# Performance work log

Hardware: AMD Instinct MI355X
Metric: run time of the kernel (lower is better)

Reference implementation:

```python
import jax, jax.numpy as jnp
import numpy as np

B, NUM_CLASSES, H, W, CF = 2, 19, 64, 64, 256
TOPK_IDX = 20  # hard-coded in the torch source: sorted descending value at index 20


def _cosine(x):
    # x: [B, N, D] -> clamped cosine affinity [B, N, N]
    xn = x / (jnp.linalg.norm(x, axis=2, keepdims=True) + 1e-9)
    return jnp.maximum(jnp.einsum('bnd,bmd->bnm', xn, xn), 0.0)


def _conv1x1(x, w, b):
    # x: [B, C, H, W], w: [O, C], b: [O]
    return jnp.einsum('bchw,oc->bohw', x, w) + b[None, :, None, None]


def setup_inputs() -> dict:
    key = jax.random.key(0)
    ks = jax.random.split(key, 12)
    s_c = (2.0 / NUM_CLASSES) ** 0.5  # kaiming fan_in scale for 1x1 conv
    s_f = (2.0 / CF) ** 0.5
    return {
        'pred': jax.random.normal(ks[0], (B, NUM_CLASSES, H, W), jnp.float32),
        'feat': jax.random.normal(ks[1], (B, CF, H, W), jnp.float32),
        'w_cls1': jax.random.normal(ks[2], (NUM_CLASSES, NUM_CLASSES), jnp.float32) * s_c,
        'b_cls1': jnp.zeros((NUM_CLASSES,), jnp.float32),
        'w_cls2': jax.random.normal(ks[3], (NUM_CLASSES, NUM_CLASSES), jnp.float32) * s_c,
        'b_cls2': jnp.zeros((NUM_CLASSES,), jnp.float32),
        'w_pro1': jax.random.normal(ks[4], (CF, CF), jnp.float32) * s_f,
        'b_pro1': jnp.zeros((CF,), jnp.float32),
        'w_pro2': jax.random.normal(ks[5], (CF, CF), jnp.float32) * s_f,
        'b_pro2': jnp.zeros((CF,), jnp.float32),
        'class_weight': jnp.ones((NUM_CLASSES,), jnp.float32),
    }


def reference(pred, feat, w_cls1, b_cls1, w_cls2, b_cls2,
              w_pro1, b_pro1, w_pro2, b_pro2, class_weight):
    bsz, c, h, w = feat.shape
    C = pred.shape[1]
    N = h * w
    feat_flat = feat.reshape(bsz, c, N).transpose(0, 2, 1)  # [B, N, 256]

    # --- no_grad block 1: confidence mask + top-k sparsified cosine affinity ---
    prob = jax.nn.softmax(pred, axis=1)
    p_prob = prob.max(axis=1)      # [B, H, W]
    p_max = prob.argmax(axis=1)    # [B, H, W]
    cwm = class_weight / (class_weight.max() + 1e-10) * 0.95
    mask = ((p_prob >= 0.95) | (p_prob >= cwm[p_max])).astype(jnp.float32)
    mask = jax.lax.stop_gradient(mask.reshape(bsz, N, 1))  # broadcast over classes

    aff1 = _cosine(feat_flat)                                # [B, N, N]
    thr = -jnp.sort(-aff1, axis=-1)[:, :, TOPK_IDX:TOPK_IDX + 1]  # per-row 21st largest
    aff1 = jnp.where(aff1 < thr, 0.0, aff1)
    aff1 = jax.lax.stop_gradient(aff1 + aff1.transpose(0, 2, 1))

    # --- degree-normalized propagation of predictions ---
    pred_flat = pred.reshape(bsz, C, N).transpose(0, 2, 1)   # [B, N, C]
    d1 = (aff1.sum(-1) + 1e-10) ** -0.5                      # D^{-1/2}
    aff1n = d1[:, :, None] * aff1 * d1[:, None, :]           # D^{-1/2} A D^{-1/2}
    p2 = jnp.einsum('bnm,bmc->bnc', aff1n, pred_flat)
    p3 = (0.8 * p2 + 0.2 * pred_flat) * (1.0 - mask) + (0.2 * p2 + 0.8 * pred_flat) * mask
    pred2 = p3.transpose(0, 2, 1).reshape(bsz, C, h, w)
    pred_out = _conv1x1(_conv1x1(pred2, w_cls1, b_cls1), w_cls2, b_cls2)

    # --- no_grad block 2: class-consistency-masked affinity over refined softmax ---
    oh = jax.nn.one_hot(p_max, C, dtype=jnp.float32)         # [B, H, W, C]
    # faithful to torch: permute(0,2,3,1) on the already-[B,H,W,C] one-hot, then flat view
    oh = jnp.transpose(oh, (0, 2, 3, 1)).reshape(bsz, -1, C)
    sp = jax.nn.softmax(pred_out, axis=1).reshape(bsz, C, N).transpose(0, 2, 1)
    aff_f = _cosine(sp)
    aff_f = jnp.where(_cosine(oh) == 0.0, 0.0, aff_f)
    d2 = (aff_f.sum(-1) + 1e-10) ** -0.5
    aff_fn = jax.lax.stop_gradient(d2[:, :, None] * aff_f * d2[:, None, :])

    # --- propagate features and project ---
    new_feat = jnp.einsum('bnm,bmc->bnc', aff_fn, feat_flat)
    new_feat = new_feat.transpose(0, 2, 1).reshape(bsz, c, h, w)
    feat_out = _conv1x1(jax.nn.relu(_conv1x1(new_feat, w_pro1, b_pro1)), w_pro2, b_pro2)
    return pred_out, feat_out
```

## Files before the change

### kernel.cpp

```cpp
#include <hip/hip_runtime.h>

#define NN 4096
#define DD 256
#define CC 19
#define BB 2
#define KSPLIT 4

typedef __attribute__((ext_vector_type(8))) short bf16x8;
typedef _Float16 f16x8 __attribute__((ext_vector_type(8)));
typedef __attribute__((ext_vector_type(4))) float f32x4;

__device__ inline unsigned short f2b(float f) {
  unsigned int u = __float_as_uint(f);
  return (unsigned short)((u + 0x7FFFu + ((u >> 16) & 1u)) >> 16);
}
__device__ inline float b2f(unsigned short h) {
  return __uint_as_float(((unsigned int)h) << 16);
}
__device__ inline unsigned int pack2(float a, float b) {
  return (unsigned int)f2b(a) | ((unsigned int)f2b(b) << 16);
}
__device__ inline void split16(float x, unsigned short& h, unsigned short& l) {
  _Float16 hh = (_Float16)x;
  float hf = (float)hh;
  _Float16 ll = (_Float16)((x - hf) * 2048.0f);
  h = *reinterpret_cast<unsigned short*>(&hh);
  l = *reinterpret_cast<unsigned short*>(&ll);
}

__global__ void k_mask_bits(const float* __restrict__ pred, const float* __restrict__ cw,
                            float* __restrict__ maskb, unsigned int* __restrict__ ohbits) {
  int g = blockIdx.x * 256 + threadIdx.x;
  if (g >= BB * NN) return;
  int b = g >> 12, n = g & (NN - 1);
  const float* p = pred + (size_t)b * CC * NN + n;
  float v[CC];
  float mx = -1e30f; int am = 0;
#pragma unroll
  for (int c = 0; c < CC; ++c) {
    float t = p[(size_t)c * NN];
    v[c] = t;
    if (t > mx) { mx = t; am = c; }
  }
  float s = 0.f;
#pragma unroll
  for (int c = 0; c < CC; ++c) s += expf(v[c] - mx);
  float pprob = 1.f / s;
  float cmax = 0.f;
#pragma unroll
  for (int c = 0; c < CC; ++c) cmax = fmaxf(cmax, cw[c]);
  float cwm = cw[am] / (cmax + 1e-10f) * 0.95f;
  maskb[g] = (pprob >= 0.95f || pprob >= cwm) ? 1.f : 0.f;
  int h = n >> 6, w = n & 63;
  int L = w * (CC * 64) + am * 64 + h;
  atomicOr(&ohbits[b * NN + L / CC], 1u << (L % CC));
}

__global__ void k_norm_feat(const float* __restrict__ feat,
                            unsigned short* __restrict__ xh, unsigned short* __restrict__ xl) {
  int g = blockIdx.x * 64 + threadIdx.x;
  int b = g >> 12, n = g & (NN - 1);
  const float* f = feat + (size_t)b * DD * NN + n;
  float s = 0.f;
  for (int d = 0; d < DD; ++d) { float t = f[(size_t)d * NN]; s += t * t; }
  float r = 1.f / (sqrtf(s) + 1e-9f);
  size_t ob = ((size_t)b * NN + n) * DD;
  for (int d = 0; d < DD; d += 4) {
    ushort4 oh, ol;
    split16(f[(size_t)d * NN] * r, oh.x, ol.x);
    split16(f[(size_t)(d + 1) * NN] * r, oh.y, ol.y);
    split16(f[(size_t)(d + 2) * NN] * r, oh.z, ol.z);
    split16(f[(size_t)(d + 3) * NN] * r, oh.w, ol.w);
    *reinterpret_cast<ushort4*>(&xh[ob + d]) = oh;
    *reinterpret_cast<ushort4*>(&xl[ob + d]) = ol;
  }
}

__global__ __launch_bounds__(256, 2) void k_gram1(const unsigned short* __restrict__ xh,
                                                  const unsigned short* __restrict__ xl,
                                                  float* __restrict__ M) {
  int L = blockIdx.x;
  int b = blockIdx.y;
  int I = 0;
  while (L >= 32 - I) { L -= 32 - I; ++I; }
  int J = I + L;
  int i0 = I * 128, j0 = J * 128;
  float* Mb = M + (size_t)b * NN * NN;
  const unsigned short* XH = xh + (size_t)b * NN * DD;
  const unsigned short* XL = xl + (size_t)b * NN * DD;
  __shared__ unsigned short stage[4 * 128 * 40];
  int t = threadIdx.x;
  int wave = t >> 6, lane = t & 63;
  int wr = (wave & 1) * 64, wc = (wave >> 1) * 64;
  int lrow = lane & 15, quad = lane >> 4;
  f32x4 accH[4][4] = {}, accL[4][4] = {};
  const unsigned short* src = (wave == 0) ? XH + (size_t)i0 * DD
                             : (wave == 1) ? XL + (size_t)i0 * DD
                             : (wave == 2) ? XH + (size_t)j0 * DD
                                           : XL + (size_t)j0 * DD;
  for (int k0 = 0; k0 < DD; k0 += 32) {
#pragma unroll
    for (int e = 0; e < 8; ++e) {
      int row = lane + 64 * (e & 1);
      int o = e >> 1;
      *reinterpret_cast<int4*>(&stage[(wave * 128 + row) * 40 + o * 8]) =
          *reinterpret_cast<const int4*>(&src[(size_t)row * DD + k0 + o * 8]);
    }
    __syncthreads();
    f16x8 ah[4], al[4], bh[4], bl[4];
#pragma unroll
    for (int i = 0; i < 4; ++i) {
      int ra = wr + i * 16 + lrow;
      int rb = wc + i * 16 + lrow;
      ah[i] = *reinterpret_cast<const f16x8*>(&stage[(0 * 128 + ra) * 40 + quad * 8]);
      al[i] = *reinterpret_cast<const f16x8*>(&stage[(1 * 128 + ra) * 40 + quad * 8]);
      bh[i] = *reinterpret_cast<const f16x8*>(&stage[(2 * 128 + rb) * 40 + quad * 8]);
      bl[i] = *reinterpret_cast<const f16x8*>(&stage[(3 * 128 + rb) * 40 + quad * 8]);
    }
#pragma unroll
    for (int i = 0; i < 4; ++i) {
#pragma unroll
      for (int j = 0; j < 4; ++j) {
        accH[i][j] = __builtin_amdgcn_mfma_f32_16x16x32_f16(ah[i], bh[j], accH[i][j], 0, 0, 0);
        accL[i][j] = __builtin_amdgcn_mfma_f32_16x16x32_f16(ah[i], bl[j], accL[i][j], 0, 0, 0);
        accL[i][j] = __builtin_amdgcn_mfma_f32_16x16x32_f16(al[i], bh[j], accL[i][j], 0, 0, 0);
      }
    }
    __syncthreads();
  }
#pragma unroll
  for (int i = 0; i < 4; ++i)
#pragma unroll
    for (int j = 0; j < 4; ++j)
#pragma unroll
      for (int reg = 0; reg < 4; ++reg)
        accH[i][j][reg] = fmaxf(accH[i][j][reg] + accL[i][j][reg] * 4.8828125e-4f, 0.f);
  float* buf = (float*)stage;
  int rr = t >> 4, cc = t & 15;
  for (int half = 0; half < 2; ++half) {
    __syncthreads();
    if ((wr >> 6) == half) {
#pragma unroll
      for (int i = 0; i < 4; ++i)
#pragma unroll
        for (int j = 0; j < 4; ++j)
#pragma unroll
          for (int reg = 0; reg < 4; ++reg)
            buf[(i * 16 + quad * 4 + reg) * 132 + wc + j * 16 + lrow] = accH[i][j][reg];
    }
    __syncthreads();
#pragma unroll
    for (int i = 0; i < 4; ++i) {
      int row = rr + i * 16;
#pragma unroll
      for (int q = 0; q < 2; ++q) {
        int col = cc * 4 + q * 64;
        *reinterpret_cast<float4*>(&Mb[(size_t)(i0 + half * 64 + row) * NN + j0 + col]) =
            *reinterpret_cast<float4*>(&buf[row * 132 + col]);
      }
    }
  }
  if (I != J) {
    for (int half = 0; half < 2; ++half) {
      __syncthreads();
      if ((wc >> 6) == half) {
#pragma unroll
        for (int i = 0; i < 4; ++i)
#pragma unroll
          for (int j = 0; j < 4; ++j)
#pragma unroll
            for (int reg = 0; reg < 4; ++reg)
              buf[(j * 16 + lrow) * 132 + wr + i * 16 + quad * 4 + reg] = accH[i][j][reg];
      }
      __syncthreads();
#pragma unroll
      for (int i = 0; i < 4; ++i) {
        int row = rr + i * 16;
#pragma unroll
        for (int q = 0; q < 2; ++q) {
          int col = cc * 4 + q * 64;
          *reinterpret_cast<float4*>(&Mb[(size_t)(j0 + half * 64 + row) * NN + i0 + col]) =
              *reinterpret_cast<float4*>(&buf[row * 132 + col]);
        }
      }
    }
  }
}

__global__ __launch_bounds__(256, 2) void k_topk(const float* __restrict__ M,
                                                 float* __restrict__ thr) {
  __shared__ unsigned int cbuf[4][64];
  int b = blockIdx.y;
  int wave = threadIdx.x >> 6, lane = threadIdx.x & 63;
  int n = blockIdx.x * 4 + wave;
  const float* row = M + (size_t)b * NN * NN + (size_t)n * NN;
  uint4 v[16];
#pragma unroll
  for (int e = 0; e < 16; ++e) {
    unsigned long long addr = (unsigned long long)(row + lane * 4 + e * 256);
    asm volatile("global_load_dwordx4 %0, %1, off" : "=v"(v[e]) : "v"(addr));
  }
  asm volatile("s_waitcnt vmcnt(0)" ::: "memory");
  __builtin_amdgcn_sched_barrier(0);
  unsigned int mx = 0u;
#pragma unroll
  for (int e = 0; e < 16; ++e) {
    unsigned int a = v[e].x > v[e].y ? v[e].x : v[e].y;
    unsigned int c2 = v[e].z > v[e].w ? v[e].z : v[e].w;
    a = a > c2 ? a : c2;
    mx = mx > a ? mx : a;
  }
  unsigned int lo = 0u, hi = 0x3FC00000u;
  while (lo < hi) {
    unsigned int mid = lo + ((hi - lo + 1) >> 1);
    if (__popcll(__ballot(mx >= mid)) >= 21) lo = mid; else hi = mid - 1;
  }
  unsigned int s = lo;
  unsigned int base = 0;
  unsigned long long ltmask = (1ull << lane) - 1ull;
#pragma unroll
  for (int e = 0; e < 16; ++e) {
#pragma unroll
    for (int q = 0; q < 4; ++q) {
      unsigned int val = (q == 0) ? v[e].x : (q == 1) ? v[e].y : (q == 2) ? v[e].z : v[e].w;
      unsigned long long mk = __ballot(val >= s);
      if (mk) {
        unsigned int pos = base + (unsigned int)__popcll(mk & ltmask);
        if (val >= s && pos < 64u) cbuf[wave][pos] = val;
        base += (unsigned int)__popcll(mk);
      }
    }
  }
  asm volatile("s_waitcnt lgkmcnt(0)" ::: "memory");
  __builtin_amdgcn_sched_barrier(0);
  unsigned int t = s;
  if (base <= 64u) {
    unsigned int cand = (lane < (int)base) ? cbuf[wave][lane] : 0u;
    lo = s; hi = 0x3FC00000u;
    while (lo < hi) {
      unsigned int mid = lo + ((hi - lo + 1) >> 1);
      if (__popcll(__ballot(cand >= mid)) >= 21) lo = mid; else hi = mid - 1;
    }
    t = lo;
  }
  {
    unsigned int t1 = t + 1u;
    int c1 = 0, c2 = 0;
#pragma unroll
    for (int e = 0; e < 16; ++e) {
      c1 += (int)__popcll(__ballot(v[e].x >= t));
      c1 += (int)__popcll(__ballot(v[e].y >= t));
      c1 += (int)__popcll(__ballot(v[e].z >= t));
      c1 += (int)__popcll(__ballot(v[e].w >= t));
      c2 += (int)__popcll(__ballot(v[e].x >= t1));
      c2 += (int)__popcll(__ballot(v[e].y >= t1));
      c2 += (int)__popcll(__ballot(v[e].z >= t1));
      c2 += (int)__popcll(__ballot(v[e].w >= t1));
    }
    if (!(c1 >= 21 && c2 < 21)) {
      lo = 0u; hi = 0x40000000u;
      while (lo < hi) {
        unsigned int mid = lo + ((hi - lo + 1) >> 1);
        int c = 0;
#pragma unroll
        for (int e = 0; e < 16; ++e) {
          c += (int)__popcll(__ballot(v[e].x >= mid));
          c += (int)__popcll(__ballot(v[e].y >= mid));
          c += (int)__popcll(__ballot(v[e].z >= mid));
          c += (int)__popcll(__ballot(v[e].w >= mid));
        }
        if (c >= 21) lo = mid; else hi = mid - 1;
      }
      t = lo;
    }
  }
  if (lane == 0) thr[b * NN + n] = __uint_as_float(t);
}

__global__ __launch_bounds__(256) void k_symm(float* __restrict__ M, const float* __restrict__ thr,
                                              float* __restrict__ dsum) {
  int L = blockIdx.x;
  int b = blockIdx.y;
  int I = 0;
  while (L >= 64 - I) { L -= 64 - I; ++I; }
  int J = I + L;
  float* Mb = M + (size_t)b * NN * NN;
  unsigned short* Mus = (unsigned short*)Mb;
  const float* th = thr + b * NN;
  __shared__ float A[64][65];
  int t = threadIdx.x;
  int i0 = I * 64, j0 = J * 64;
  float areg[16];
#pragma unroll
  for (int e = 0; e < 16; ++e) {
    int lin = t + e * 256;
    int i = lin >> 6, j = lin & 63;
    areg[e] = Mb[(size_t)(i0 + i) * NN + j0 + j];
  }
#pragma unroll
  for (int e = 0; e < 16; ++e) {
    int lin = t + e * 256;
    int i = lin >> 6, j = lin & 63;
    float a = areg[e];
    float v = a * ((a >= th[i0 + i] ? 1.f : 0.f) + (a >= th[j0 + j] ? 1.f : 0.f));
    A[i][j] = v;
  }
  __syncthreads();
  {
    int i = t >> 2, seg = (t & 3) * 16;
    float v[16];
#pragma unroll
    for (int q = 0; q < 4; ++q)
      *reinterpret_cast<float4*>(&v[q * 4]) = *reinterpret_cast<float4*>(&A[i][seg + q * 4]);
    unsigned int pk[8];
#pragma unroll
    for (int q = 0; q < 8; ++q) pk[q] = pack2(v[2 * q], v[2 * q + 1]);
    size_t ub = 2 * (size_t)(i0 + i) * NN + 2 * (size_t)j0 + seg;
    *reinterpret_cast<int4*>(&Mus[ub])     = *reinterpret_cast<int4*>(&pk[0]);
    *reinterpret_cast<int4*>(&Mus[ub + 8]) = *reinterpret_cast<int4*>(&pk[4]);
  }
  if (I != J) {
    int j = t >> 2, seg = (t & 3) * 16;
    float v[16];
#pragma unroll
    for (int e = 0; e < 16; ++e) v[e] = A[seg + e][j];
    unsigned int pk[8];
#pragma unroll
    for (int q = 0; q < 8; ++q) pk[q] = pack2(v[2 * q], v[2 * q + 1]);
    size_t ub = 2 * (size_t)(j0 + j) * NN + 2 * (size_t)i0 + seg;
    *reinterpret_cast<int4*>(&Mus[ub])     = *reinterpret_cast<int4*>(&pk[0]);
    *reinterpret_cast<int4*>(&Mus[ub + 8]) = *reinterpret_cast<int4*>(&pk[4]);
  }
  if (t < 64) {
    float s = 0.f;
#pragma unroll
    for (int j = 0; j < 64; ++j) s += A[t][j];
    atomicAdd(&dsum[b * NN + i0 + t], s);
  } else if (t < 128 && I != J) {
    int j = t - 64;
    float s = 0.f;
#pragma unroll
    for (int i = 0; i < 64; ++i) s += A[i][j];
    atomicAdd(&dsum[b * NN + j0 + j], s);
  }
}

__global__ void k_fin_d(float* __restrict__ d) {
  int g = blockIdx.x * 256 + threadIdx.x;
  if (g < BB * NN) d[g] = 1.f / sqrtf(d[g] + 1e-10f);
}

__global__ void k_make_yb(const float* __restrict__ pred, const float* __restrict__ d1,
                          unsigned short* __restrict__ ybh) {
  int g = blockIdx.x * 256 + threadIdx.x;
  int idx = g * 4;
  int b = idx / (32 * NN);
  int c = (idx / NN) & 31;
  int n = idx & (NN - 1);
  ushort4 o = make_ushort4(0, 0, 0, 0);
  if (c < CC) {
    float4 p = *reinterpret_cast<const float4*>(&pred[((size_t)b * CC + c) * NN + n]);
    const float* dd = d1 + b * NN + n;
    o.x = f2b(p.x * dd[0]); o.y = f2b(p.y * dd[1]);
    o.z = f2b(p.z * dd[2]); o.w = f2b(p.w * dd[3]);
  }
  *reinterpret_cast<ushort4*>(&ybh[idx]) = o;
}

__global__ __launch_bounds__(256) void k_p2_mfma(
    const float* __restrict__ M, const unsigned short* __restrict__ ybh,
    const float* __restrict__ d1, float* __restrict__ p2b) {
  int b = blockIdx.y;
  int n0 = blockIdx.x * 64;
  const unsigned short* Mus = (const unsigned short*)(M + (size_t)b * NN * NN);
  const unsigned short* Y = ybh + (size_t)b * 32 * NN;
  __shared__ unsigned short As[64][72];
  __shared__ unsigned short Ys[32][72];
  int t = threadIdx.x;
  int wave = t >> 6, lane = t & 63;
  int wn = (wave & 1) * 32;
  int wc = (wave >> 1) * 16;
  int lrow = lane & 15, quad = lane >> 4;
  f32x4 acc[2] = {{0.f,0.f,0.f,0.f},{0.f,0.f,0.f,0.f}};
  int sr = t >> 3, scc = (t & 7) * 8;
  for (int m0 = 0; m0 < NN; m0 += 64) {
#pragma unroll
    for (int e = 0; e < 2; ++e) {
      int rr = sr + e * 32;
      *reinterpret_cast<int4*>(&As[rr][scc]) =
          *reinterpret_cast<const int4*>(&Mus[2 * (size_t)(n0 + rr) * NN + 2 * (size_t)m0 + scc]);
    }
    *reinterpret_cast<int4*>(&Ys[sr][scc]) =
        *reinterpret_cast<const int4*>(&Y[(size_t)sr * NN + m0 + scc]);
    __syncthreads();
#pragma unroll
    for (int kc = 0; kc < 2; ++kc) {
      int ko = kc * 32 + quad * 8;
      bf16x8 bfr = *reinterpret_cast<const bf16x8*>(&Ys[wc + lrow][ko]);
#pragma unroll
      for (int i = 0; i < 2; ++i) {
        bf16x8 af = *reinterpret_cast<const bf16x8*>(&As[wn + i * 16 + lrow][ko]);
        acc[i] = __builtin_amdgcn_mfma_f32_16x16x32_bf16(af, bfr, acc[i], 0, 0, 0);
      }
    }
    __syncthreads();
  }
  int c = wc + lrow;
  if (c < CC) {
#pragma unroll
    for (int i = 0; i < 2; ++i) {
#pragma unroll
      for (int reg = 0; reg < 4; ++reg) {
        int n = n0 + wn + i * 16 + quad * 4 + reg;
        p2b[((size_t)b * NN + n) * CC + c] = d1[b * NN + n] * acc[i][reg];
      }
    }
  }
}

__global__ __launch_bounds__(256) void k_pred_head(const float* __restrict__ pred,
    const float* __restrict__ p2b, const float* __restrict__ maskb,
    const float* __restrict__ w1, const float* __restrict__ b1,
    const float* __restrict__ w2, const float* __restrict__ b2,
    float* __restrict__ out, float* __restrict__ spnT) {
  __shared__ float sw1[CC * CC], sw2[CC * CC], sb1[CC], sb2[CC];
  int t = threadIdx.x;
  for (int i = t; i < CC * CC; i += 256) { sw1[i] = w1[i]; sw2[i] = w2[i]; }
  if (t < CC) { sb1[t] = b1[t]; sb2[t] = b2[t]; }
  __syncthreads();
  int g = blockIdx.x * 256 + t;
  int b = g >> 12, n = g & (NN - 1);
  float m = maskb[g];
  float ca = (m > 0.5f) ? 0.2f : 0.8f;
  float cb = (m > 0.5f) ? 0.8f : 0.2f;
  const float* P = pred + (size_t)b * CC * NN + n;
  const float* Q = p2b + (size_t)g * CC;
  float p3[CC];
#pragma unroll
  for (int c = 0; c < CC; ++c) p3[c] = ca * Q[c] + cb * P[(size_t)c * NN];
  float midv[CC];
#pragma unroll
  for (int o = 0; o < CC; ++o) {
    float s = sb1[o];
#pragma unroll
    for (int c = 0; c < CC; ++c) s += sw1[o * CC + c] * p3[c];
    midv[o] = s;
  }
  float ov[CC];
  float mx = -1e30f;
#pragma unroll
  for (int o = 0; o < CC; ++o) {
    float s = sb2[o];
#pragma unroll
    for (int c = 0; c < CC; ++c) s += sw2[o * CC + c] * midv[c];
    ov[o] = s;
    out[(size_t)b * CC * NN + (size_t)o * NN + n] = s;
    mx = fmaxf(mx, s);
  }
  float se = 0.f;
  float e[CC];
#pragma unroll
  for (int o = 0; o < CC; ++o) { e[o] = expf(ov[o] - mx); se += e[o]; }
  float inv = 1.f / se;
  float nrm = 0.f;
#pragma unroll
  for (int o = 0; o < CC; ++o) { float sp = e[o] * inv; e[o] = sp; nrm += sp * sp; }
  float rn = 1.f / (sqrtf(nrm) + 1e-9f);
#pragma unroll
  for (int o = 0; o < CC; ++o) spnT[(size_t)b * CC * NN + (size_t)o * NN + n] = e[o] * rn;
}

__global__ __launch_bounds__(256) void k_gram2(const float* __restrict__ spnT,
    const unsigned int* __restrict__ bits, unsigned short* __restrict__ Mh) {
  int L = blockIdx.x;
  int b = blockIdx.y;
  int I = 0;
  while (L >= 64 - I) { L -= 64 - I; ++I; }
  int J = I + L;
  const float* X = spnT + (size_t)b * CC * NN;
  unsigned short* Mb = Mh + (size_t)b * NN * NN;
  __shared__ float sA[CC][64], sB[CC][64];
  __shared__ unsigned int bI[64], bJ[64];
  __shared__ float tr[64][65];
  int t = threadIdx.x;
  int r = t >> 4, c = t & 15;
  int i0 = I * 64, j0 = J * 64;
  for (int e = t; e < CC * 64; e += 256) {
    int k = e >> 6, col = e & 63;
    sA[k][col] = X[(size_t)k * NN + i0 + col];
    sB[k][col] = X[(size_t)k * NN + j0 + col];
  }
  if (t < 64) bI[t] = bits[b * NN + i0 + t];
  else if (t < 128) bJ[t - 64] = bits[b * NN + j0 + t - 64];
  __syncthreads();
  float acc[4][4] = {};
#pragma unroll
  for (int k = 0; k < CC; ++k) {
    float av[4], bv[4];
#pragma unroll
    for (int i = 0; i < 4; ++i) av[i] = sA[k][r * 4 + i];
#pragma unroll
    for (int j = 0; j < 4; ++j) bv[j] = sB[k][c * 4 + j];
#pragma unroll
    for (int i = 0; i < 4; ++i) {
#pragma unroll
      for (int j = 0; j < 4; ++j) acc[i][j] += av[i] * bv[j];
    }
  }
#pragma unroll
  for (int i = 0; i < 4; ++i) {
#pragma unroll
    for (int j = 0; j < 4; ++j) {
      bool keep = (bI[r * 4 + i] & bJ[c * 4 + j]) != 0u;
      acc[i][j] = keep ? fmaxf(acc[i][j], 0.f) : 0.f;
    }
    ushort4 v;
    v.x = f2b(acc[i][0]); v.y = f2b(acc[i][1]); v.z = f2b(acc[i][2]); v.w = f2b(acc[i][3]);
    *reinterpret_cast<ushort4*>(&Mb[(size_t)(i0 + r * 4 + i) * NN + j0 + c * 4]) = v;
  }
  if (I != J) {
#pragma unroll
    for (int i = 0; i < 4; ++i) {
#pragma unroll
      for (int j = 0; j < 4; ++j) tr[r * 4 + i][c * 4 + j] = acc[i][j];
    }
    __syncthreads();
#pragma unroll
    for (int e = 0; e < 16; ++e) {
      int lin = t + e * 256;
      int jr = lin >> 6, ic = lin & 63;
      Mb[(size_t)(j0 + jr) * NN + i0 + ic] = f2b(tr[ic][jr]);
    }
  }
}

__global__ __launch_bounds__(256) void k_rowsum2h(const unsigned short* __restrict__ Mh,
                                                  float* __restrict__ d2) {
  int b = blockIdx.y, n = blockIdx.x;
  const unsigned short* row = Mh + (size_t)b * NN * NN + (size_t)n * NN;
  int t = threadIdx.x;
  float s = 0.f;
#pragma unroll
  for (int i = 0; i < 8; ++i) {
    unsigned int u = *reinterpret_cast<const unsigned int*>(&row[(i * 256 + t) * 2]);
    s += __uint_as_float(u << 16) + __uint_as_float(u & 0xffff0000u);
  }
  for (int off = 32; off > 0; off >>= 1) s += __shfl_down(s, off);
  __shared__ float p4[4];
  int wid = t >> 6, lane = t & 63;
  if (lane == 0) p4[wid] = s;
  __syncthreads();
  if (t == 0) d2[b * NN + n] = 1.f / sqrtf(p4[0] + p4[1] + p4[2] + p4[3] + 1e-10f);
}

__global__ void k_make_z(const float* __restrict__ feat, const float* __restrict__ d2,
                         unsigned short* __restrict__ zb) {
  int g = blockIdx.x * 256 + threadIdx.x;
  int idx = g * 4;
  int b = idx / (DD * NN);
  int m = idx & (NN - 1);
  float4 f = *reinterpret_cast<const float4*>(&feat[idx]);
  const float* dd = d2 + b * NN + m;
  ushort4 o;
  o.x = f2b(f.x * dd[0]); o.y = f2b(f.y * dd[1]);
  o.z = f2b(f.z * dd[2]); o.w = f2b(f.w * dd[3]);
  *reinterpret_cast<ushort4*>(&zb[idx]) = o;
}

__global__ void k_prep_w(const float* __restrict__ w1, const float* __restrict__ w2,
                         unsigned short* __restrict__ wb1, unsigned short* __restrict__ wb2) {
  int g = blockIdx.x * 256 + threadIdx.x;
  wb1[g] = f2b(w1[g]);
  wb2[g] = f2b(w2[g]);
}

__global__ __launch_bounds__(256) void k_newfeat_mfma(
    const unsigned short* __restrict__ Mh, const unsigned short* __restrict__ zb,
    float* __restrict__ nfp) {
  int zz = blockIdx.z;
  int b = zz / KSPLIT, ks = zz % KSPLIT;
  int nblk = blockIdx.x;
  int dblk = blockIdx.y;
  const int KLEN = NN / KSPLIT;
  const unsigned short* A = zb + (size_t)b * DD * NN + (size_t)(dblk * 64) * NN + ks * KLEN;
  const unsigned short* Bm = Mh + (size_t)b * NN * NN + (size_t)(nblk * 64) * NN + ks * KLEN;
  __shared__ unsigned short As[64][72];
  __shared__ unsigned short Bs[64][72];
  int t = threadIdx.x;
  int wave = t >> 6, lane = t & 63;
  int wd = (wave & 1) * 32, wn = (wave >> 1) * 32;
  int lrow = lane & 15, quad = lane >> 4;
  f32x4 acc[2][2] = {{{0.f,0.f,0.f,0.f},{0.f,0.f,0.f,0.f}},{{0.f,0.f,0.f,0.f},{0.f,0.f,0.f,0.f}}};
  int sr = t >> 3, sc = (t & 7) * 8;
  for (int m0 = 0; m0 < KLEN; m0 += 64) {
#pragma unroll
    for (int e = 0; e < 2; ++e) {
      int rr = sr + e * 32;
      *reinterpret_cast<int4*>(&As[rr][sc]) =
          *reinterpret_cast<const int4*>(&A[(size_t)rr * NN + m0 + sc]);
      *reinterpret_cast<int4*>(&Bs[rr][sc]) =
          *reinterpret_cast<const int4*>(&Bm[(size_t)rr * NN + m0 + sc]);
    }
    __syncthreads();
#pragma unroll
    for (int kc = 0; kc < 2; ++kc) {
      int ko = kc * 32 + quad * 8;
      bf16x8 af[2], bfr[2];
#pragma unroll
      for (int i = 0; i < 2; ++i) {
        af[i]  = *reinterpret_cast<const bf16x8*>(&As[wd + i * 16 + lrow][ko]);
        bfr[i] = *reinterpret_cast<const bf16x8*>(&Bs[wn + i * 16 + lrow][ko]);
      }
#pragma unroll
      for (int i = 0; i < 2; ++i)
#pragma unroll
        for (int j = 0; j < 2; ++j)
          acc[i][j] = __builtin_amdgcn_mfma_f32_16x16x32_bf16(af[i], bfr[j], acc[i][j], 0, 0, 0);
    }
    __syncthreads();
  }
#pragma unroll
  for (int j = 0; j < 2; ++j) {
    int n = nblk * 64 + wn + j * 16 + lrow;
#pragma unroll
    for (int i = 0; i < 2; ++i) {
      int d = dblk * 64 + wd + i * 16 + quad * 4;
      float4 v = make_float4(acc[i][j].x, acc[i][j].y, acc[i][j].z, acc[i][j].w);
      *reinterpret_cast<float4*>(&nfp[((size_t)zz * NN + n) * DD + d]) = v;
    }
  }
}

__global__ void k_nf_reduce(const float* __restrict__ nfp, const float* __restrict__ d2,
                            unsigned short* __restrict__ nfh) {
  int g = blockIdx.x * 256 + threadIdx.x;
  int idx = g * 4;
  int b = idx / (NN * DD);
  int n = (idx / DD) & (NN - 1);
  size_t base = (size_t)idx + (size_t)b * (KSPLIT - 1) * NN * DD;
  float4 s = make_float4(0.f, 0.f, 0.f, 0.f);
#pragma unroll
  for (int ks = 0; ks < KSPLIT; ++ks) {
    float4 v = *reinterpret_cast<const float4*>(&nfp[base + (size_t)ks * NN * DD]);
    s.x += v.x; s.y += v.y; s.z += v.z; s.w += v.w;
  }
  float sc = d2[b * NN + n];
  ushort4 o;
  o.x = f2b(s.x * sc); o.y = f2b(s.y * sc); o.z = f2b(s.z * sc); o.w = f2b(s.w * sc);
  *reinterpret_cast<ushort4*>(&nfh[idx]) = o;
}

__global__ __launch_bounds__(256) void k_conv1_mfma(
    const unsigned short* __restrict__ nfh, const unsigned short* __restrict__ wb1,
    const float* __restrict__ b1, unsigned short* __restrict__ midh) {
  int b = blockIdx.z;
  int nblk = blockIdx.x;
  int oblk = blockIdx.y;
  int n0 = nblk * 64, o0 = oblk * 64;
  __shared__ unsigned short As[64][72];
  __shared__ unsigned short Bs[64][72];
  int t = threadIdx.x;
  int wave = t >> 6, lane = t & 63;
  int wn = (wave & 1) * 32, wo = (wave >> 1) * 32;
  int lrow = lane & 15, quad = lane >> 4;
  f32x4 acc[2][2] = {{{0.f,0.f,0.f,0.f},{0.f,0.f,0.f,0.f}},{{0.f,0.f,0.f,0.f},{0.f,0.f,0.f,0.f}}};
  int sr = t >> 3, sc = (t & 7) * 8;
  for (int d0 = 0; d0 < DD; d0 += 64) {
#pragma unroll
    for (int e = 0; e < 2; ++e) {
      int rr = sr + e * 32;
      *reinterpret_cast<int4*>(&As[rr][sc]) =
          *reinterpret_cast<const int4*>(&nfh[((size_t)b * NN + n0 + rr) * DD + d0 + sc]);
      *reinterpret_cast<int4*>(&Bs[rr][sc]) =
          *reinterpret_cast<const int4*>(&wb1[(size_t)(o0 + rr) * DD + d0 + sc]);
    }
    __syncthreads();
#pragma unroll
    for (int kc = 0; kc < 2; ++kc) {
      int ko = kc * 32 + quad * 8;
      bf16x8 af[2], bfr[2];
#pragma unroll
      for (int i = 0; i < 2; ++i) {
        af[i]  = *reinterpret_cast<const bf16x8*>(&As[wn + i * 16 + lrow][ko]);
        bfr[i] = *reinterpret_cast<const bf16x8*>(&Bs[wo + i * 16 + lrow][ko]);
      }
#pragma unroll
      for (int i = 0; i < 2; ++i)
#pragma unroll
        for (int j = 0; j < 2; ++j)
          acc[i][j] = __builtin_amdgcn_mfma_f32_16x16x32_bf16(af[i], bfr[j], acc[i][j], 0, 0, 0);
    }
    __syncthreads();
  }
#pragma unroll
  for (int j = 0; j < 2; ++j) {
    int o = o0 + wo + j * 16 + lrow;
    float bias = b1[o];
#pragma unroll
    for (int i = 0; i < 2; ++i) {
      int nb = n0 + wn + i * 16 + quad * 4;
      ushort4 v;
      v.x = f2b(fmaxf(acc[i][j].x + bias, 0.f));
      v.y = f2b(fmaxf(acc[i][j].y + bias, 0.f));
      v.z = f2b(fmaxf(acc[i][j].z + bias, 0.f));
      v.w = f2b(fmaxf(acc[i][j].w + bias, 0.f));
      *reinterpret_cast<ushort4*>(&midh[((size_t)b * DD + o) * NN + nb]) = v;
    }
  }
}

__global__ __launch_bounds__(256) void k_conv2_mfma(
    const unsigned short* __restrict__ midh, const unsigned short* __restrict__ wb2,
    const float* __restrict__ b2, float* __restrict__ outp) {
  int b = blockIdx.z;
  int nblk = blockIdx.x;
  int oblk = blockIdx.y;
  int n0 = nblk * 64, o0 = oblk * 64;
  __shared__ unsigned short As[64][72];
  __shared__ unsigned short Bs[64][72];
  int t = threadIdx.x;
  int wave = t >> 6, lane = t & 63;
  int wn = (wave & 1) * 32, wo = (wave >> 1) * 32;
  int lrow = lane & 15, quad = lane >> 4;
  f32x4 acc[2][2] = {{{0.f,0.f,0.f,0.f},{0.f,0.f,0.f,0.f}},{{0.f,0.f,0.f,0.f},{0.f,0.f,0.f,0.f}}};
  int sr = t >> 3, sc = (t & 7) * 8;
  for (int d0 = 0; d0 < DD; d0 += 64) {
#pragma unroll
    for (int e = 0; e < 2; ++e) {
      int rr = sr + e * 32;
      *reinterpret_cast<int4*>(&Bs[rr][sc]) =
          *reinterpret_cast<const int4*>(&wb2[(size_t)(o0 + rr) * DD + d0 + sc]);
      unsigned short v[8];
      *reinterpret_cast<int4*>(v) =
          *reinterpret_cast<const int4*>(&midh[((size_t)b * DD + d0 + rr) * NN + n0 + sc]);
#pragma unroll
      for (int j = 0; j < 8; ++j) As[sc + j][rr] = v[j];
    }
    __syncthreads();
#pragma unroll
    for (int kc = 0; kc < 2; ++kc) {
      int ko = kc * 32 + quad * 8;
      bf16x8 af[2], bfr[2];
#pragma unroll
      for (int i = 0; i < 2; ++i) {
        af[i]  = *reinterpret_cast<const bf16x8*>(&As[wn + i * 16 + lrow][ko]);
        bfr[i] = *reinterpret_cast<const bf16x8*>(&Bs[wo + i * 16 + lrow][ko]);
      }
#pragma unroll
      for (int i = 0; i < 2; ++i)
#pragma unroll
        for (int j = 0; j < 2; ++j)
          acc[i][j] = __builtin_amdgcn_mfma_f32_16x16x32_bf16(af[i], bfr[j], acc[i][j], 0, 0, 0);
    }
    __syncthreads();
  }
#pragma unroll
  for (int j = 0; j < 2; ++j) {
    int o = o0 + wo + j * 16 + lrow;
    float bias = b2[o];
#pragma unroll
    for (int i = 0; i < 2; ++i) {
      int nb = n0 + wn + i * 16 + quad * 4;
      float4 v = make_float4(acc[i][j].x + bias, acc[i][j].y + bias,
                             acc[i][j].z + bias, acc[i][j].w + bias);
      *reinterpret_cast<float4*>(&outp[((size_t)b * DD + o) * NN + nb]) = v;
    }
  }
}

extern "C" void kernel_launch(void* const* d_in, const int* in_sizes, int n_in,
                              void* d_out, int out_size, void* d_ws, size_t ws_size,
                              hipStream_t stream) {
  (void)in_sizes; (void)n_in; (void)out_size; (void)ws_size;
  const float* pred   = (const float*)d_in[0];
  const float* feat   = (const float*)d_in[1];
  const float* w_cls1 = (const float*)d_in[2];
  const float* b_cls1 = (const float*)d_in[3];
  const float* w_cls2 = (const float*)d_in[4];
  const float* b_cls2 = (const float*)d_in[5];
  const float* w_pro1 = (const float*)d_in[6];
  const float* b_pro1 = (const float*)d_in[7];
  const float* w_pro2 = (const float*)d_in[8];
  const float* b_pro2 = (const float*)d_in[9];
  const float* cw     = (const float*)d_in[10];
  float* out = (float*)d_out;

  float* Mbuf = (float*)d_ws;
  float* spnT = Mbuf + (size_t)BB * NN * NN;
  float* p2b  = spnT + (size_t)BB * CC * NN;
  float* thr  = p2b + (size_t)BB * NN * CC;
  float* dsum = thr + BB * NN;
  float* d2s  = dsum + BB * NN;
  float* maskb = d2s + BB * NN;
  unsigned int* ohbits = (unsigned int*)(maskb + BB * NN);
  unsigned short* xh   = (unsigned short*)(ohbits + BB * NN);
  unsigned short* xl   = xh + (size_t)BB * NN * DD;
  unsigned short* nfh  = xl + (size_t)BB * NN * DD;
  unsigned short* midh = nfh + (size_t)BB * NN * DD;
  unsigned short* zb   = midh + (size_t)BB * DD * NN;
  unsigned short* wb1  = zb + (size_t)BB * DD * NN;
  unsigned short* wb2  = wb1 + (size_t)DD * DD;
  unsigned short* ybh  = wb2 + (size_t)DD * DD;
  unsigned short* Mh   = (unsigned short*)Mbuf;
  float* nfp = (float*)(Mh + (size_t)BB * NN * NN);

  hipMemsetAsync(dsum, 0, sizeof(float) * BB * NN, stream);
  hipMemsetAsync(ohbits, 0, sizeof(unsigned int) * BB * NN, stream);

  k_mask_bits<<<BB * NN / 256, 256, 0, stream>>>(pred, cw, maskb, ohbits);
  k_norm_feat<<<BB * NN / 64, 64, 0, stream>>>(feat, xh, xl);
  k_gram1<<<dim3(528, BB), 256, 0, stream>>>(xh, xl, Mbuf);
  k_topk<<<dim3(NN / 4, BB), 256, 0, stream>>>(Mbuf, thr);
  k_symm<<<dim3(2080, BB), 256, 0, stream>>>(Mbuf, thr, dsum);
  k_fin_d<<<BB * NN / 256, 256, 0, stream>>>(dsum);
  k_make_yb<<<BB * 32 * NN / 4 / 256, 256, 0, stream>>>(pred, dsum, ybh);
  k_p2_mfma<<<dim3(NN / 64, BB), 256, 0, stream>>>(Mbuf, ybh, dsum, p2b);
  k_pred_head<<<BB * NN / 256, 256, 0, stream>>>(pred, p2b, maskb, w_cls1, b_cls1,
                                                 w_cls2, b_cls2, out, spnT);
  k_gram2<<<dim3(2080, BB), 256, 0, stream>>>(spnT, ohbits, Mh);
  k_rowsum2h<<<dim3(NN, BB), 256, 0, stream>>>(Mh, d2s);
  k_make_z<<<BB * DD * NN / 4 / 256, 256, 0, stream>>>(feat, d2s, zb);
  k_prep_w<<<DD * DD / 256, 256, 0, stream>>>(w_pro1, w_pro2, wb1, wb2);
  k_newfeat_mfma<<<dim3(64, 4, BB * KSPLIT), 256, 0, stream>>>(Mh, zb, nfp);
  k_nf_reduce<<<BB * NN * DD / 4 / 256, 256, 0, stream>>>(nfp, d2s, nfh);
  k_conv1_mfma<<<dim3(64, 4, BB), 256, 0, stream>>>(nfh, wb1, b_pro1, midh);
  k_conv2_mfma<<<dim3(64, 4, BB), 256, 0, stream>>>(midh, wb2, b_pro2,
                                                    out + (size_t)BB * CC * NN);
}
```

Before: 398.6 us.

## Double-buffer gram1 staging with direct global-to-LDS loads and XOR swizzle

The gram kernel's K-loop now uses global_load_lds to copy tiles straight into LDS and double-buffers the stage array, so the next K slice is prefetched while MFMAs run on the current one. The padded LDS layout is replaced by an unpadded 32-wide layout with an XOR swizzle on the 16-byte chunk index to avoid bank conflicts. This doubles LDS use and relies on the async LDS loads being complete by the single barrier per iteration. There is no explicit vmcnt wait, so correctness depends on the compiler inserting one.

New measurement: 385.5 us. 1.03x faster.

```diff
diff --git a/kernel.cpp b/kernel.cpp
--- a/kernel.cpp
+++ b/kernel.cpp
@@ -9,6 +9,10 @@
 typedef __attribute__((ext_vector_type(8))) short bf16x8;
 typedef _Float16 f16x8 __attribute__((ext_vector_type(8)));
 typedef __attribute__((ext_vector_type(4))) float f32x4;
+
+#define GLL16(gp, lp) __builtin_amdgcn_global_load_lds( \
+    (const __attribute__((address_space(1))) unsigned int*)(gp), \
+    (__attribute__((address_space(3))) unsigned int*)(lp), 16, 0, 0)
 
 __device__ inline unsigned short f2b(float f) {
   unsigned int u = __float_as_uint(f);
@@ -88,34 +92,41 @@
   float* Mb = M + (size_t)b * NN * NN;
   const unsigned short* XH = xh + (size_t)b * NN * DD;
   const unsigned short* XL = xl + (size_t)b * NN * DD;
-  __shared__ unsigned short stage[4 * 128 * 40];
+  __shared__ unsigned short stage[2][4][128][32];
   int t = threadIdx.x;
   int wave = t >> 6, lane = t & 63;
   int wr = (wave & 1) * 64, wc = (wave >> 1) * 64;
   int lrow = lane & 15, quad = lane >> 4;
+  int sel = (lrow >> 1) & 3;
   f32x4 accH[4][4] = {}, accL[4][4] = {};
   const unsigned short* src = (wave == 0) ? XH + (size_t)i0 * DD
                              : (wave == 1) ? XL + (size_t)i0 * DD
                              : (wave == 2) ? XH + (size_t)j0 * DD
                                            : XL + (size_t)j0 * DD;
+  int srow = lane >> 2;
+  int spart = (lane & 3) ^ ((lane >> 3) & 3);
+#pragma unroll
+  for (int e = 0; e < 8; ++e)
+    GLL16(&src[(size_t)(e * 16 + srow) * DD + spart * 8], &stage[0][wave][e * 16][0]);
+  __syncthreads();
+  int cur = 0;
   for (int k0 = 0; k0 < DD; k0 += 32) {
-#pragma unroll
-    for (int e = 0; e < 8; ++e) {
-      int row = lane + 64 * (e & 1);
-      int o = e >> 1;
-      *reinterpret_cast<int4*>(&stage[(wave * 128 + row) * 40 + o * 8]) =
-          *reinterpret_cast<const int4*>(&src[(size_t)row * DD + k0 + o * 8]);
-    }
-    __syncthreads();
+    if (k0 + 32 < DD) {
+#pragma unroll
+      for (int e = 0; e < 8; ++e)
+        GLL16(&src[(size_t)(e * 16 + srow) * DD + k0 + 32 + spart * 8],
+              &stage[cur ^ 1][wave][e * 16][0]);
+    }
     f16x8 ah[4], al[4], bh[4], bl[4];
 #pragma unroll
     for (int i = 0; i < 4; ++i) {
       int ra = wr + i * 16 + lrow;
       int rb = wc + i * 16 + lrow;
-      ah[i] = *reinterpret_cast<const f16x8*>(&stage[(0 * 128 + ra) * 40 + quad * 8]);
-      al[i] = *reinterpret_cast<const f16x8*>(&stage[(1 * 128 + ra) * 40 + quad * 8]);
-      bh[i] = *reinterpret_cast<const f16x8*>(&stage[(2 * 128 + rb) * 40 + quad * 8]);
-      bl[i] = *reinterpret_cast<const f16x8*>(&stage[(3 * 128 + rb) * 40 + quad * 8]);
+      int sl = (quad ^ sel) * 8;
+      ah[i] = *reinterpret_cast<const f16x8*>(&stage[cur][0][ra][sl]);
+      al[i] = *reinterpret_cast<const f16x8*>(&stage[cur][1][ra][sl]);
+      bh[i] = *reinterpret_cast<const f16x8*>(&stage[cur][2][rb][sl]);
+      bl[i] = *reinterpret_cast<const f16x8*>(&stage[cur][3][rb][sl]);
     }
 #pragma unroll
     for (int i = 0; i < 4; ++i) {
@@ -127,6 +138,7 @@
       }
     }
     __syncthreads();
+    cur ^= 1;
   }
 #pragma unroll
   for (int i = 0; i < 4; ++i)
```
